# Performance work log

Hardware: AMD Instinct MI355X
Metric: run time of the kernel (lower is better)

## Reference

```python
import jax, jax.numpy as jnp
import numpy as np

NQ = 8
NL = 3
DIM = 2 ** NQ


def _rx(psi, w, theta):
    # theta: scalar or [B]
    B = psi.shape[0]
    t = jnp.atleast_1d(theta).astype(jnp.float32)
    c = jnp.cos(t / 2)[:, None, None].astype(jnp.complex64)
    s = (-1j * jnp.sin(t / 2))[:, None, None].astype(jnp.complex64)
    p = psi.reshape(B, 2 ** w, 2, -1)
    s0, s1 = p[:, :, 0], p[:, :, 1]
    return jnp.stack([c * s0 + s * s1, s * s0 + c * s1], axis=2).reshape(B, DIM)


def _ry(psi, w, theta):
    B = psi.shape[0]
    t = jnp.atleast_1d(theta).astype(jnp.float32)
    c = jnp.cos(t / 2)[:, None, None].astype(jnp.complex64)
    s = jnp.sin(t / 2)[:, None, None].astype(jnp.complex64)
    p = psi.reshape(B, 2 ** w, 2, -1)
    s0, s1 = p[:, :, 0], p[:, :, 1]
    return jnp.stack([c * s0 - s * s1, s * s0 + c * s1], axis=2).reshape(B, DIM)


def _rz(psi, w, theta):
    B = psi.shape[0]
    t = jnp.atleast_1d(theta).astype(jnp.float32)
    e0 = jnp.exp(-0.5j * t.astype(jnp.complex64))[:, None, None]
    e1 = jnp.exp(0.5j * t.astype(jnp.complex64))[:, None, None]
    p = psi.reshape(B, 2 ** w, 2, -1)
    return jnp.stack([e0 * p[:, :, 0], e1 * p[:, :, 1]], axis=2).reshape(B, DIM)


def _cnot(psi, c, t):
    # control c, target t (wire 0 = most significant axis)
    B = psi.shape[0]
    a, b = (c, t) if c < t else (t, c)
    p = psi.reshape(B, 2 ** a, 2, 2 ** (b - a - 1), 2, -1)
    caxis = 2 if c < t else 4
    taxis = 4 if c < t else 2
    idx = [slice(None)] * 6
    idx[caxis] = 1
    sub = p[tuple(idx)]  # control=1 slab, caxis removed
    fl_axis = taxis - (1 if taxis > caxis else 0)
    p = p.at[tuple(idx)].set(jnp.flip(sub, axis=fl_axis))
    return p.reshape(B, DIM)


# PauliZ signs per wire: [NQ, 2^NQ]
_bits = (np.arange(DIM)[None, :] >> (NQ - 1 - np.arange(NQ)[:, None])) & 1
_Z_SIGNS = jnp.asarray((1 - 2 * _bits).astype(np.float32))


def _quantum_layer(enc, qrx, qry, qrz):
    # enc: [B, NQ] encoding angles; qrx/qry/qrz: [NL, NQ] scalar params
    B = enc.shape[0]
    psi = jnp.zeros((B, DIM), jnp.complex64).at[:, 0].set(1.0)
    for i in range(NQ):
        psi = _rx(psi, i, enc[:, i])
    for l in range(NL):
        for i in range(NQ):
            psi = _rx(psi, i, qrx[l, i])
            psi = _ry(psi, i, qry[l, i])
            psi = _rz(psi, i, qrz[l, i])
        for i in range(NQ - 1):
            psi = _cnot(psi, i, i + 1)
        psi = _cnot(psi, NQ - 1, 0)
    probs = psi.real ** 2 + psi.imag ** 2  # [B, 2^NQ]
    return probs @ _Z_SIGNS.T  # [B, NQ] <Z_i>


def _critic(x, w1, b1, w2, b2, qrx, qry, qrz, w3, b3, w4, b4):
    h = jax.nn.relu(x @ w1 + b1)
    enc = h @ w2 + b2
    ex = _quantum_layer(enc, qrx, qry, qrz)
    h2 = jax.nn.relu(ex @ w3 + b3)
    return h2 @ w4 + b4


def setup_inputs() -> dict:
    key = jax.random.key(0)
    ks = jax.random.split(key, 32)
    B, OBS, ACT, H = 65536, 96, 32, 256
    D = OBS + ACT

    def lin(k, fin, fout):
        return jax.random.normal(k, (fin, fout), jnp.float32) * (1.0 / np.sqrt(fin))

    inp = {
        'state': jax.random.normal(ks[0], (B, OBS), jnp.float32),
        'action': jax.random.normal(ks[1], (B, ACT), jnp.float32),
    }
    for ci, tag in enumerate(['a', 'b']):
        o = 2 + ci * 15
        inp['w1' + tag] = lin(ks[o + 0], D, H)
        inp['b1' + tag] = jnp.zeros((H,), jnp.float32)
        inp['w2' + tag] = lin(ks[o + 1], H, NQ)
        inp['b2' + tag] = jnp.zeros((NQ,), jnp.float32)
        inp['qrx' + tag] = jax.random.normal(ks[o + 2], (NL, NQ), jnp.float32)
        inp['qry' + tag] = jax.random.normal(ks[o + 3], (NL, NQ), jnp.float32)
        inp['qrz' + tag] = jax.random.normal(ks[o + 4], (NL, NQ), jnp.float32)
        inp['w3' + tag] = lin(ks[o + 5], NQ, H)
        inp['b3' + tag] = jnp.zeros((H,), jnp.float32)
        inp['w4' + tag] = lin(ks[o + 6], H, 1)
        inp['b4' + tag] = jnp.zeros((1,), jnp.float32)
    return inp


def reference(state, action,
              w1a, b1a, w2a, b2a, qrxa, qrya, qrza, w3a, b3a, w4a, b4a,
              w1b, b1b, w2b, b2b, qrxb, qryb, qrzb, w3b, b3b, w4b, b4b):
    x = jnp.concatenate([state, action], axis=1)
    q1 = _critic(x, w1a, b1a, w2a, b2a, qrxa, qrya, qrza, w3a, b3a, w4a, b4a)
    q2 = _critic(x, w1b, b1b, w2b, b2b, qrxb, qryb, qrzb, w3b, b3b, w4b, b4b)
    return (q1, q2)
```

## Files before the change

### kernel.cpp

```cpp
#include <hip/hip_runtime.h>
#include <math.h>


typedef __attribute__((ext_vector_type(8))) short bfrag_t;
typedef __attribute__((ext_vector_type(16))) float accv_t;

__device__ __forceinline__ unsigned short f2bf(float x) {
  unsigned u = __float_as_uint(x);
  u += 0x7FFFu + ((u >> 16) & 1u);
  return (unsigned short)(u >> 16);
}
__device__ __forceinline__ float bf2f(unsigned short h) {
  return __uint_as_float(((unsigned)h) << 16);
}
__device__ __forceinline__ unsigned pack2(float a, float b) {
  return (unsigned)f2bf(a) | ((unsigned)f2bf(b) << 16);
}

struct C2 { float r, i; };
__device__ __forceinline__ C2 cmul(C2 a, C2 b){ return C2{a.r*b.r - a.i*b.i, a.r*b.i + a.i*b.r}; }
__device__ __forceinline__ C2 cadd(C2 a, C2 b){ return C2{a.r+b.r, a.i+b.i}; }

#define APPLY2(A,Bx)                                                        \
  { float ar=re[A], ai=im[A], br=re[Bx], bi=im[Bx];                         \
    re[A]  = u00r*ar - u00i*ai + u01r*br - u01i*bi;                         \
    im[A]  = u00r*ai + u00i*ar + u01r*bi + u01i*br;                         \
    re[Bx] = u10r*ar - u10i*ai + u11r*br - u11i*bi;                         \
    im[Bx] = u10r*ai + u10i*ar + u11r*bi + u11i*br; }

__global__ __launch_bounds__(256)
void prep_weights(const float* __restrict__ qrxa, const float* __restrict__ qrya,
                  const float* __restrict__ qrza,
                  const float* __restrict__ qrxb, const float* __restrict__ qryb,
                  const float* __restrict__ qrzb,
                  const float* __restrict__ w1a, const float* __restrict__ w1b,
                  const float* __restrict__ w2a, const float* __restrict__ w2b,
                  const float* __restrict__ w3a, const float* __restrict__ w3b,
                  unsigned short* __restrict__ Bm, unsigned short* __restrict__ Gm,
                  unsigned short* __restrict__ w1p, unsigned short* __restrict__ w2p) {
  int blk = blockIdx.x;
  int tid = threadIdx.x;
  if (blk < 128) {
    __shared__ float sg[192];
    int c = blk >> 6;
    if (tid < 24) {
      const float* qx = c ? qrxb : qrxa;
      const float* qy = c ? qryb : qrya;
      const float* qz = c ? qrzb : qrza;
      int g = tid;
      float tx = 0.5f*qx[g], ty = 0.5f*qy[g], tz = 0.5f*qz[g];
      float cx = cosf(tx), sx = sinf(tx);
      float cy = cosf(ty), sy = sinf(ty);
      float cz = cosf(tz), sz = sinf(tz);
      C2 rx00{cx,0.f}, rx01{0.f,-sx}, rx10{0.f,-sx}, rx11{cx,0.f};
      C2 m00 = cadd(cmul(C2{cy,0.f},rx00), cmul(C2{-sy,0.f},rx10));
      C2 m01 = cadd(cmul(C2{cy,0.f},rx01), cmul(C2{-sy,0.f},rx11));
      C2 m10 = cadd(cmul(C2{sy,0.f},rx00), cmul(C2{cy,0.f},rx10));
      C2 m11 = cadd(cmul(C2{sy,0.f},rx01), cmul(C2{cy,0.f},rx11));
      C2 e0{cz,-sz}, e1{cz,sz};
      C2 u00 = cmul(e0,m00), u01 = cmul(e0,m01), u10 = cmul(e1,m10), u11 = cmul(e1,m11);
      float* o = sg + g*8;
      o[0]=u00.r; o[1]=u00.i; o[2]=u01.r; o[3]=u01.i;
      o[4]=u10.r; o[5]=u10.i; o[6]=u11.r; o[7]=u11.i;
    }
    __syncthreads();
    int lane = tid & 63;
    int wid = blk*4 + (tid >> 6);
    int bcol = wid & 255;
    int p = __popc(bcol) & 3;
    float phr = (p==0) ? 1.f : ((p==2) ? -1.f : 0.f);
    float phi = (p==1) ? -1.f : ((p==3) ? 1.f : 0.f);
    float re[4], im[4];
    #pragma unroll
    for (int j = 0; j < 4; ++j) {
      int idx = 4*lane + j;
      re[j] = (idx==bcol) ? phr : 0.f;
      im[j] = (idx==bcol) ? phi : 0.f;
    }
    #pragma unroll
    for (int l = 0; l < 3; ++l) {
      #pragma unroll
      for (int q = 0; q < 8; ++q) {
        const float* u = &sg[(size_t)(l*8 + q)*8];
        float u00r=u[0],u00i=u[1],u01r=u[2],u01i=u[3];
        float u10r=u[4],u10i=u[5],u11r=u[6],u11i=u[7];
        if (q < 6) {
          int m = 5-q, mask = 1<<m;
          bool s1 = ((lane >> m) & 1) != 0;
          float udr = s1?u11r:u00r, udi = s1?u11i:u00i;
          float uor = s1?u10r:u01r, uoi = s1?u10i:u01i;
          #pragma unroll
          for (int j = 0; j < 4; ++j) {
            float pr = __shfl_xor(re[j], mask);
            float pi = __shfl_xor(im[j], mask);
            float nr = udr*re[j] - udi*im[j] + uor*pr - uoi*pi;
            float ni = udr*im[j] + udi*re[j] + uor*pi + uoi*pr;
            re[j]=nr; im[j]=ni;
          }
        } else if (q == 6) { APPLY2(0,2); APPLY2(1,3); }
        else               { APPLY2(0,1); APPLY2(2,3); }
      }
      #pragma unroll
      for (int cq = 0; cq <= 4; ++cq) {
        int tmask = 1 << (4-cq);
        bool pred = ((lane >> (5-cq)) & 1) != 0;
        #pragma unroll
        for (int j = 0; j < 4; ++j) {
          float sr = __shfl_xor(re[j], tmask);
          float si = __shfl_xor(im[j], tmask);
          re[j] = pred ? sr : re[j];
          im[j] = pred ? si : im[j];
        }
      }
      { bool pred = (lane & 1) != 0;
        float t0, t1;
        t0 = pred?re[2]:re[0]; t1 = pred?re[0]:re[2]; re[0]=t0; re[2]=t1;
        t0 = pred?im[2]:im[0]; t1 = pred?im[0]:im[2]; im[0]=t0; im[2]=t1;
        t0 = pred?re[3]:re[1]; t1 = pred?re[1]:re[3]; re[1]=t0; re[3]=t1;
        t0 = pred?im[3]:im[1]; t1 = pred?im[1]:im[3]; im[1]=t0; im[3]=t1; }
      { float t;
        t=re[2]; re[2]=re[3]; re[3]=t;
        t=im[2]; im[2]=im[3]; im[3]=t; }
      { re[1]=__shfl_xor(re[1],32); im[1]=__shfl_xor(im[1],32);
        re[3]=__shfl_xor(re[3],32); im[3]=__shfl_xor(im[3],32); }
    }
    #pragma unroll
    for (int j = 0; j < 4; ++j) {
      int i = 4*lane + j;
      Bm[(size_t)(c*512 + i)*256 + bcol]       = f2bf(re[j]);
      Bm[(size_t)(c*512 + 256 + i)*256 + bcol] = f2bf(im[j]);
    }
  } else if (blk < 192) {
    int slot = (blk-128)*256 + tid;
    int n = slot & 255, h5 = (slot>>8)&1, ks = (slot>>9)&7, p = (slot>>12)&1, c = slot>>13;
    const float* w1c = c ? w1b : w1a;
    #pragma unroll
    for (int j = 0; j < 8; ++j) {
      float v = w1c[(size_t)(ks*16 + h5*8 + j)*256 + n];
      unsigned short hi = f2bf(v);
      w1p[(size_t)slot*8 + j] = p ? f2bf(v - bf2f(hi)) : hi;
    }
  } else if (blk < 200) {
    int slot = (blk-192)*256 + tid;
    int combo = slot >> 4, part = slot & 15;
    int h5 = combo&1, k16 = (combo>>1)&15, p = (combo>>5)&1, c = (combo>>6)&1;
    const float* w2c = c ? w2b : w2a;
    #pragma unroll
    for (int jj = 0; jj < 16; ++jj) {
      int idx = part*16 + jj;
      int il = idx >> 3, j = idx & 7;
      int n = k16*16 + h5*8 + j;
      float v = (il < 8) ? w2c[(size_t)n*8 + il] : 0.f;
      unsigned short hi = f2bf(v);
      w2p[(size_t)combo*256 + idx] = p ? f2bf(v - bf2f(hi)) : hi;
    }
  } else {
    int idx = (blk-200)*256 + tid;
    int j = idx & 7, lane = (idx >> 3) & 63, w = (idx >> 9) & 7, c = (idx >> 12) & 1;
    int h5 = lane >> 5, il = lane & 31;
    int n = 32*w + il;
    const float* w3 = c ? w3b : w3a;
    Gm[idx] = h5 ? (unsigned short)0 : f2bf(w3[j*256 + n]);
  }
}

__global__ __launch_bounds__(256, 4)
void enc_mfma(const float* __restrict__ state, const float* __restrict__ action,
              const unsigned short* __restrict__ w1p,
              const float* __restrict__ b1a, const float* __restrict__ b1b,
              const unsigned short* __restrict__ w2p,
              const float* __restrict__ b2a, const float* __restrict__ b2b,
              float* __restrict__ enc, int Bn) {
  __shared__ __align__(16) char Bx[2][8192];
  __shared__ __align__(16) float sb1[2][256];
  __shared__ float sb2[2][8];
  __shared__ __align__(16) float encw[4][32][8];
  int tid = threadIdx.x;
  int lane = tid & 63, w = tid >> 6, il = lane & 31, h5 = lane >> 5;
  int r0 = blockIdx.x * 32;

  sb1[0][tid] = b1a[tid];
  sb1[1][tid] = b1b[tid];
  if (tid < 8) { sb2[0][tid] = b2a[tid]; sb2[1][tid] = b2b[tid]; }

  {
    int m = tid >> 3, q8 = tid & 7;
    const float4* st4 = (const float4*)state;
    const float4* ac4 = (const float4*)action;
    #pragma unroll
    for (int j = 0; j < 4; ++j) {
      int f = j*8 + q8;
      int ks = f >> 2, kq = f & 3;
      float4 v = (ks < 6) ? st4[(size_t)(r0+m)*24 + ks*4 + kq]
                          : ac4[(size_t)(r0+m)*8 + (ks-6)*4 + kq];
      unsigned short hx = f2bf(v.x), hy = f2bf(v.y), hz = f2bf(v.z), hw = f2bf(v.w);
      uint2 hh, ll;
      hh.x = (unsigned)hx | ((unsigned)hy << 16);
      hh.y = (unsigned)hz | ((unsigned)hw << 16);
      ll.x = (unsigned)f2bf(v.x - bf2f(hx)) | ((unsigned)f2bf(v.y - bf2f(hy)) << 16);
      ll.y = (unsigned)f2bf(v.z - bf2f(hz)) | ((unsigned)f2bf(v.w - bf2f(hw)) << 16);
      int off = ks*1024 + m*32 + kq*8;
      *(uint2*)(&Bx[0][off]) = hh;
      *(uint2*)(&Bx[1][off]) = ll;
    }
  }
  __syncthreads();

  for (int c = 0; c < 2; ++c) {
    accv_t A[2] = {{},{}};
    #pragma unroll
    for (int ks = 0; ks < 8; ++ks) {
      bfrag_t a0h, a0l, a1h, a1l;
      {
        size_t b0 = ((size_t)((c*2+0)*8 + ks)*2 + h5)*256;
        size_t b1 = ((size_t)((c*2+1)*8 + ks)*2 + h5)*256;
        int t0 = 2*w, t1 = 2*w+1;
        a0h = *(const bfrag_t*)(w1p + (b0 + t0*32 + il)*8);
        a0l = *(const bfrag_t*)(w1p + (b1 + t0*32 + il)*8);
        a1h = *(const bfrag_t*)(w1p + (b0 + t1*32 + il)*8);
        a1l = *(const bfrag_t*)(w1p + (b1 + t1*32 + il)*8);
      }
      bfrag_t b0h = *(const bfrag_t*)(&Bx[0][ks*1024 + il*32 + h5*16]);
      bfrag_t b0l = *(const bfrag_t*)(&Bx[1][ks*1024 + il*32 + h5*16]);
      A[0] = __builtin_amdgcn_mfma_f32_32x32x16_bf16(a0h, b0h, A[0], 0,0,0);
      A[0] = __builtin_amdgcn_mfma_f32_32x32x16_bf16(a0h, b0l, A[0], 0,0,0);
      A[0] = __builtin_amdgcn_mfma_f32_32x32x16_bf16(a0l, b0h, A[0], 0,0,0);
      A[1] = __builtin_amdgcn_mfma_f32_32x32x16_bf16(a1h, b0h, A[1], 0,0,0);
      A[1] = __builtin_amdgcn_mfma_f32_32x32x16_bf16(a1h, b0l, A[1], 0,0,0);
      A[1] = __builtin_amdgcn_mfma_f32_32x32x16_bf16(a1l, b0h, A[1], 0,0,0);
    }
    #pragma unroll
    for (int nt = 0; nt < 2; ++nt) {
      #pragma unroll
      for (int g = 0; g < 4; ++g) {
        float4 bb = *(const float4*)&sb1[c][(2*w+nt)*32 + 8*g + 4*h5];
        float bba[4] = {bb.x, bb.y, bb.z, bb.w};
        #pragma unroll
        for (int jj = 0; jj < 4; ++jj) {
          A[nt][4*g+jj] = fmaxf(A[nt][4*g+jj] + bba[jj], 0.f);
        }
      }
    }
    accv_t Cm = {};
    #pragma unroll
    for (int k2 = 0; k2 < 4; ++k2) {
      int k16 = 4*w + k2;
      bfrag_t g2h = *(const bfrag_t*)(w2p + ((size_t)((c*2+0)*16 + k16)*2 + h5)*256 + il*8);
      bfrag_t g2l = *(const bfrag_t*)(w2p + ((size_t)((c*2+1)*16 + k16)*2 + h5)*256 + il*8);
      unsigned ph[2][2], pl[2][2];
      #pragma unroll
      for (int gi = 0; gi < 2; ++gi) {
        int G = 2*k2 + gi, nt = G >> 2, g = G & 3;
        float f0 = A[nt][4*g+0], f1 = A[nt][4*g+1];
        float f2 = A[nt][4*g+2], f3 = A[nt][4*g+3];
        unsigned short h0 = f2bf(f0), h1 = f2bf(f1), h2 = f2bf(f2), h3 = f2bf(f3);
        ph[gi][0] = (unsigned)h0 | ((unsigned)h1 << 16);
        ph[gi][1] = (unsigned)h2 | ((unsigned)h3 << 16);
        pl[gi][0] = (unsigned)f2bf(f0 - bf2f(h0)) | ((unsigned)f2bf(f1 - bf2f(h1)) << 16);
        pl[gi][1] = (unsigned)f2bf(f2 - bf2f(h2)) | ((unsigned)f2bf(f3 - bf2f(h3)) << 16);
      }
      union { bfrag_t v; unsigned u[4]; } FH, FL;
      #pragma unroll
      for (int r = 0; r < 2; ++r) {
        unsigned own_h = h5 ? ph[1][r] : ph[0][r];
        unsigned alt_h = h5 ? ph[0][r] : ph[1][r];
        unsigned rec_h = __shfl_xor((int)alt_h, 32);
        FH.u[r]   = h5 ? rec_h : own_h;
        FH.u[2+r] = h5 ? own_h : rec_h;
        unsigned own_l = h5 ? pl[1][r] : pl[0][r];
        unsigned alt_l = h5 ? pl[0][r] : pl[1][r];
        unsigned rec_l = __shfl_xor((int)alt_l, 32);
        FL.u[r]   = h5 ? rec_l : own_l;
        FL.u[2+r] = h5 ? own_l : rec_l;
      }
      Cm = __builtin_amdgcn_mfma_f32_32x32x16_bf16(g2h, FH.v, Cm, 0,0,0);
      Cm = __builtin_amdgcn_mfma_f32_32x32x16_bf16(g2h, FL.v, Cm, 0,0,0);
      Cm = __builtin_amdgcn_mfma_f32_32x32x16_bf16(g2l, FH.v, Cm, 0,0,0);
    }
    *(float4*)&encw[w][il][4*h5] = make_float4(Cm[0], Cm[1], Cm[2], Cm[3]);
    __syncthreads();
    {
      int e = tid & 7, mm = tid >> 3;
      float v = sb2[c][e];
      #pragma unroll
      for (int ww = 0; ww < 4; ++ww) v += encw[ww][mm][e];
      enc[((size_t)c*Bn + r0 + mm)*8 + e] = v;
    }
    __syncthreads();
  }
}

__device__ __forceinline__ void a_build(float4 ea, float4 eb, char* Ab, int ag2, int am) {
  float c0,s0,c1,s1,c2,s2,c3,s3,c4,s4,c5,s5,c6,s6,c7,s7;
  __sincosf(0.5f*ea.x, &s0, &c0);
  __sincosf(0.5f*ea.y, &s1, &c1);
  __sincosf(0.5f*ea.z, &s2, &c2);
  __sincosf(0.5f*ea.w, &s3, &c3);
  __sincosf(0.5f*eb.x, &s4, &c4);
  __sincosf(0.5f*eb.y, &s5, &c5);
  __sincosf(0.5f*eb.z, &s6, &c6);
  __sincosf(0.5f*eb.w, &s7, &c7);
  float v0 = (ag2&8) ? s0 : c0;
  float v1 = (ag2&4) ? s1 : c1;
  float v2 = (ag2&2) ? s2 : c2;
  float v3 = (ag2&1) ? s3 : c3;
  float top = v0*v1*v2*v3;
  float hA = top*c4, hB = top*s4;
  float p67[4];
  p67[0] = c6*c7; p67[1] = c6*s7; p67[2] = s6*c7; p67[3] = s6*s7;
  float low[8];
  #pragma unroll
  for (int j = 0; j < 8; ++j) low[j] = ((j&4) ? s5 : c5) * p67[j&3];
  union { bfrag_t v; unsigned u[4]; } pk;
  #pragma unroll
  for (int k = 0; k < 4; ++k) pk.u[k] = pack2(hA*low[2*k], hA*low[2*k+1]);
  *(bfrag_t*)(Ab + ag2*1024 + am*16) = pk.v;
  #pragma unroll
  for (int k = 0; k < 4; ++k) pk.u[k] = pack2(hB*low[2*k], hB*low[2*k+1]);
  *(bfrag_t*)(Ab + ag2*1024 + 512 + am*16) = pk.v;
}

__global__ __launch_bounds__(512, 2)
void qgemm(const float* __restrict__ enc,
           const unsigned short* __restrict__ Bm, const unsigned short* __restrict__ Gm,
           const float* __restrict__ b3a, const float* __restrict__ w4a, const float* __restrict__ b4a,
           const float* __restrict__ b3b, const float* __restrict__ w4b, const float* __restrict__ b4b,
           float* __restrict__ out, int Bn) {
  __shared__ __align__(16) char APq[119808];
  char* A0 = APq;
  char* A1 = APq + 16384;
  float* exw = (float*)(APq + 32768);
  float* exf = (float*)(APq + 51200);
  float* qtmp = (float*)(APq + 54272);

  int tid = threadIdx.x;
  int lane = tid & 63;
  int w = tid >> 6;
  int il = lane & 31;
  int h5 = lane >> 5;

  int c = blockIdx.x >> 7;
  int rowblock = blockIdx.x & 127;
  int rowsPerBlock = Bn >> 7;
  int npairs = rowsPerBlock >> 6;

  bfrag_t bf0[16], bf1[16];
  {
    const unsigned short* base = Bm + ((size_t)(c*512 + 32*w + il)*256 + h5*8);
    #pragma unroll
    for (int ks = 0; ks < 16; ++ks) {
      bf0[ks] = *(const bfrag_t*)(base + ks*16);
      bf1[ks] = *(const bfrag_t*)(base + 256*256 + ks*16);
    }
  }
  bfrag_t gf2 = *(const bfrag_t*)(Gm + ((size_t)((c*8 + w)*64 + lane))*8);

  int n2 = 32*w + il;
  const float* b3c = c ? b3b : b3a;
  const float* w4c = c ? w4b : w4a;
  const float* b4c = c ? b4b : b4a;
  float b3v = b3c[n2];
  float w4v = w4c[n2];
  float b4v = b4c[0];
  int rowAdd = 4*h5;

  int am = tid & 31, ag2 = tid >> 5;
  const float* encb = enc + ((size_t)c*Bn)*8;
  int rbase = rowblock*rowsPerBlock;

  {
    const float* ep0 = encb + (size_t)(rbase + am)*8;
    float4 pa0 = *(const float4*)ep0, pb0 = *(const float4*)(ep0 + 4);
    const float* ep1 = encb + (size_t)(rbase + 32 + am)*8;
    float4 pa1 = *(const float4*)ep1, pb1 = *(const float4*)(ep1 + 4);
    a_build(pa0, pb0, A0, ag2, am);
    a_build(pa1, pb1, A1, ag2, am);
  }
  __syncthreads();

  for (int st2 = 0; st2 < npairs; ++st2) {
    int r0 = rbase + st2*64;
    #pragma unroll
    for (int sub = 0; sub < 2; ++sub) {
      const char* Asel = sub ? A1 : A0;
      accv_t acc0 = {}, acc1 = {};
      #pragma unroll
      for (int ks = 0; ks < 16; ++ks) {
        bfrag_t af = *(const bfrag_t*)(Asel + ks*1024 + lane*16);
        acc0 = __builtin_amdgcn_mfma_f32_32x32x16_bf16(bf0[ks], af, acc0, 0, 0, 0);
        acc1 = __builtin_amdgcn_mfma_f32_32x32x16_bf16(bf1[ks], af, acc1, 0, 0, 0);
      }
      float Pv[16];
      #pragma unroll
      for (int r = 0; r < 16; ++r) Pv[r] = acc0[r]*acc0[r] + acc1[r]*acc1[r];
      float E  = ((Pv[0]+Pv[1])+(Pv[2]+Pv[3])) + ((Pv[4]+Pv[5])+(Pv[6]+Pv[7]));
      float S4 = ((Pv[8]+Pv[9])+(Pv[10]+Pv[11])) + ((Pv[12]+Pv[13])+(Pv[14]+Pv[15]));
      float T  = E + S4;
      float S0 = ((Pv[1]+Pv[3])+(Pv[5]+Pv[7])) + ((Pv[9]+Pv[11])+(Pv[13]+Pv[15]));
      float S1 = ((Pv[2]+Pv[3])+(Pv[6]+Pv[7])) + ((Pv[10]+Pv[11])+(Pv[14]+Pv[15]));
      float S3 = ((Pv[4]+Pv[5])+(Pv[6]+Pv[7])) + ((Pv[12]+Pv[13])+(Pv[14]+Pv[15]));
      float e[8];
      e[7] = T - 2.f*S0;
      e[6] = T - 2.f*S1;
      e[5] = h5 ? -T : T;
      e[4] = T - 2.f*S3;
      e[3] = T - 2.f*S4;
      e[2] = (w&1) ? -T : T;
      e[1] = (w&2) ? -T : T;
      e[0] = (w&4) ? -T : T;
      #pragma unroll
      for (int q = 0; q < 8; ++q) e[q] += __shfl_xor(e[q], 32);
      if (h5 == 0) {
        float* dst = exw + sub*2304 + w*288 + il*9;
        #pragma unroll
        for (int q = 0; q < 8; ++q) dst[q] = e[q];
      }
    }
    __syncthreads();
    float4 na0, nb0, na1, nb1;
    bool more = (st2 + 1 < npairs);
    if (more) {
      const float* ep0 = encb + (size_t)(r0 + 64 + am)*8;
      na0 = *(const float4*)ep0; nb0 = *(const float4*)(ep0 + 4);
      const float* ep1 = encb + (size_t)(r0 + 96 + am)*8;
      na1 = *(const float4*)ep1; nb1 = *(const float4*)(ep1 + 4);
    }
    {
      int sub = tid >> 8, m = (tid >> 3) & 31, q = tid & 7;
      const float* ew = exw + sub*2304 + m*9 + q;
      float s = ((ew[0] + ew[288]) + (ew[2*288] + ew[3*288]))
              + ((ew[4*288] + ew[5*288]) + (ew[6*288] + ew[7*288]));
      exf[sub*384 + m*12 + q] = s;
    }
    if (more) {
      a_build(na0, nb0, A0, ag2, am);
      a_build(na1, nb1, A1, ag2, am);
    }
    __syncthreads();
    {
      union { bfrag_t v; unsigned u[4]; } fa, fb;
      if (h5 == 0) {
        const float* e0 = exf + il*12;
        float4 x0 = *(const float4*)(e0);
        float4 x1 = *(const float4*)(e0 + 4);
        fa.u[0] = pack2(x0.x, x0.y); fa.u[1] = pack2(x0.z, x0.w);
        fa.u[2] = pack2(x1.x, x1.y); fa.u[3] = pack2(x1.z, x1.w);
        const float* e1 = exf + 384 + il*12;
        float4 y0 = *(const float4*)(e1);
        float4 y1 = *(const float4*)(e1 + 4);
        fb.u[0] = pack2(y0.x, y0.y); fb.u[1] = pack2(y0.z, y0.w);
        fb.u[2] = pack2(y1.x, y1.y); fb.u[3] = pack2(y1.z, y1.w);
      } else {
        fa.u[0]=0; fa.u[1]=0; fa.u[2]=0; fa.u[3]=0;
        fb.u[0]=0; fb.u[1]=0; fb.u[2]=0; fb.u[3]=0;
      }
      accv_t acc2a = {}, acc2b = {};
      acc2a = __builtin_amdgcn_mfma_f32_32x32x16_bf16(fa.v, gf2, acc2a, 0, 0, 0);
      acc2b = __builtin_amdgcn_mfma_f32_32x32x16_bf16(fb.v, gf2, acc2b, 0, 0, 0);
      #pragma unroll
      for (int r = 0; r < 16; ++r) {
        int row = (r&3) + 8*(r>>2) + rowAdd;
        qtmp[row*256 + n2]        = fmaxf(acc2a[r] + b3v, 0.f) * w4v;
        qtmp[(32 + row)*256 + n2] = fmaxf(acc2b[r] + b3v, 0.f) * w4v;
      }
    }
    __syncthreads();
    {
      int row = tid >> 3, seg = tid & 7;
      const float* qrow = qtmp + row*256;
      float s = 0.f;
      #pragma unroll
      for (int t = 0; t < 8; ++t) {
        float4 a = *(const float4*)(qrow + t*32 + seg*4);
        s += (a.x + a.y) + (a.z + a.w);
      }
      s += __shfl_xor(s, 1);
      s += __shfl_xor(s, 2);
      s += __shfl_xor(s, 4);
      if (seg == 0) out[(size_t)c*Bn + r0 + row] = s + b4v;
    }
  }
}

extern "C" void kernel_launch(void* const* d_in, const int* in_sizes, int n_in,
                              void* d_out, int out_size, void* d_ws, size_t ws_size,
                              hipStream_t stream) {
  (void)n_in; (void)out_size; (void)ws_size;
  const float* state  = (const float*)d_in[0];
  const float* action = (const float*)d_in[1];
  const float* w1a=(const float*)d_in[2];  const float* b1a=(const float*)d_in[3];
  const float* w2a=(const float*)d_in[4];  const float* b2a=(const float*)d_in[5];
  const float* qrxa=(const float*)d_in[6]; const float* qrya=(const float*)d_in[7];
  const float* qrza=(const float*)d_in[8];
  const float* w3a=(const float*)d_in[9];  const float* b3a=(const float*)d_in[10];
  const float* w4a=(const float*)d_in[11]; const float* b4a=(const float*)d_in[12];
  const float* w1b=(const float*)d_in[13]; const float* b1b=(const float*)d_in[14];
  const float* w2b=(const float*)d_in[15]; const float* b2b=(const float*)d_in[16];
  const float* qrxb=(const float*)d_in[17];const float* qryb=(const float*)d_in[18];
  const float* qrzb=(const float*)d_in[19];
  const float* w3b=(const float*)d_in[20]; const float* b3b=(const float*)d_in[21];
  const float* w4b=(const float*)d_in[22]; const float* b4b=(const float*)d_in[23];

  int B = in_sizes[0] / 96;
  char* wsb = (char*)d_ws;
  unsigned short* Bmat = (unsigned short*)(wsb);
  unsigned short* Gmat = (unsigned short*)(wsb + 524288);
  unsigned short* w1p  = (unsigned short*)(wsb + 786432);
  unsigned short* w2p  = (unsigned short*)(wsb + 1048576);
  float* enc           = (float*)(wsb + 1114112);

  prep_weights<<<232, 256, 0, stream>>>(qrxa,qrya,qrza,qrxb,qryb,qrzb,
                                        w1a,w1b,w2a,w2b,w3a,w3b,
                                        Bmat,Gmat,w1p,w2p);
  enc_mfma<<<B/32, 256, 0, stream>>>(state,action,w1p,b1a,b1b,w2p,b2a,b2b,enc,B);
  qgemm<<<256, 512, 0, stream>>>(enc, Bmat, Gmat, b3a, w4a, b4a, b3b, w4b, b4b,
                                 (float*)d_out, B);
}
```

Baseline: 204.2 us.

## Fold w4 magnitude and b3 into Gm, reduce head in registers

```diff
diff --git a/kernel.cpp b/kernel.cpp
--- a/kernel.cpp
+++ b/kernel.cpp
@@ -36,6 +36,8 @@
                   const float* __restrict__ w1a, const float* __restrict__ w1b,
                   const float* __restrict__ w2a, const float* __restrict__ w2b,
                   const float* __restrict__ w3a, const float* __restrict__ w3b,
+                  const float* __restrict__ w4a, const float* __restrict__ w4b,
+                  const float* __restrict__ b3a, const float* __restrict__ b3b,
                   unsigned short* __restrict__ Bm, unsigned short* __restrict__ Gm,
                   unsigned short* __restrict__ w1p, unsigned short* __restrict__ w2p) {
   int blk = blockIdx.x;
@@ -160,7 +162,14 @@
     int h5 = lane >> 5, il = lane & 31;
     int n = 32*w + il;
     const float* w3 = c ? w3b : w3a;
-    Gm[idx] = h5 ? (unsigned short)0 : f2bf(w3[j*256 + n]);
+    const float* w4 = c ? w4b : w4a;
+    const float* b3 = c ? b3b : b3a;
+    float aw = fabsf(w4[n]);
+    float v;
+    if (h5 == 0)     v = w3[(size_t)j*256 + n] * aw;
+    else if (j == 0) v = b3[n] * aw;
+    else             v = 0.f;
+    Gm[idx] = f2bf(v);
   }
 }
 
@@ -326,12 +335,12 @@
            const float* __restrict__ b3a, const float* __restrict__ w4a, const float* __restrict__ b4a,
            const float* __restrict__ b3b, const float* __restrict__ w4b, const float* __restrict__ b4b,
            float* __restrict__ out, int Bn) {
-  __shared__ __align__(16) char APq[119808];
+  __shared__ __align__(16) char APq[56576];
   char* A0 = APq;
   char* A1 = APq + 16384;
   float* exw = (float*)(APq + 32768);
   float* exf = (float*)(APq + 51200);
-  float* qtmp = (float*)(APq + 54272);
+  float* qp  = (float*)(APq + 54272);
 
   int tid = threadIdx.x;
   int lane = tid & 63;
@@ -356,13 +365,11 @@
   bfrag_t gf2 = *(const bfrag_t*)(Gm + ((size_t)((c*8 + w)*64 + lane))*8);
 
   int n2 = 32*w + il;
-  const float* b3c = c ? b3b : b3a;
   const float* w4c = c ? w4b : w4a;
   const float* b4c = c ? b4b : b4a;
-  float b3v = b3c[n2];
   float w4v = w4c[n2];
   float b4v = b4c[0];
-  int rowAdd = 4*h5;
+  unsigned smask = (unsigned)__ballot(w4v < 0.f);
 
   int am = tid & 31, ag2 = tid >> 5;
   const float* encb = enc + ((size_t)c*Bn)*8;
@@ -417,6 +424,11 @@
       }
     }
     __syncthreads();
+    if (st2 > 0 && tid < 64) {
+      const float* qr = qp + tid*9;
+      float s = ((qr[0]+qr[1]) + (qr[2]+qr[3])) + ((qr[4]+qr[5]) + (qr[6]+qr[7]));
+      out[(size_t)c*Bn + (r0 - 64) + tid] = s + b4v;
+    }
     float4 na0, nb0, na1, nb1;
     bool more = (st2 + 1 < npairs);
     if (more) {
@@ -451,34 +463,35 @@
         fb.u[0] = pack2(y0.x, y0.y); fb.u[1] = pack2(y0.z, y0.w);
         fb.u[2] = pack2(y1.x, y1.y); fb.u[3] = pack2(y1.z, y1.w);
       } else {
-        fa.u[0]=0; fa.u[1]=0; fa.u[2]=0; fa.u[3]=0;
-        fb.u[0]=0; fb.u[1]=0; fb.u[2]=0; fb.u[3]=0;
+        fa.u[0] = 0x00003F80u; fa.u[1]=0; fa.u[2]=0; fa.u[3]=0;
+        fb.u[0] = 0x00003F80u; fb.u[1]=0; fb.u[2]=0; fb.u[3]=0;
       }
       accv_t acc2a = {}, acc2b = {};
-      acc2a = __builtin_amdgcn_mfma_f32_32x32x16_bf16(fa.v, gf2, acc2a, 0, 0, 0);
-      acc2b = __builtin_amdgcn_mfma_f32_32x32x16_bf16(fb.v, gf2, acc2b, 0, 0, 0);
+      acc2a = __builtin_amdgcn_mfma_f32_32x32x16_bf16(gf2, fa.v, acc2a, 0, 0, 0);
+      acc2b = __builtin_amdgcn_mfma_f32_32x32x16_bf16(gf2, fb.v, acc2b, 0, 0, 0);
+      float qa = 0.f, qb = 0.f;
       #pragma unroll
       for (int r = 0; r < 16; ++r) {
-        int row = (r&3) + 8*(r>>2) + rowAdd;
-        qtmp[row*256 + n2]        = fmaxf(acc2a[r] + b3v, 0.f) * w4v;
-        qtmp[(32 + row)*256 + n2] = fmaxf(acc2b[r] + b3v, 0.f) * w4v;
-      }
-    }
-    __syncthreads();
-    {
-      int row = tid >> 3, seg = tid & 7;
-      const float* qrow = qtmp + row*256;
-      float s = 0.f;
-      #pragma unroll
-      for (int t = 0; t < 8; ++t) {
-        float4 a = *(const float4*)(qrow + t*32 + seg*4);
-        s += (a.x + a.y) + (a.z + a.w);
-      }
-      s += __shfl_xor(s, 1);
-      s += __shfl_xor(s, 2);
-      s += __shfl_xor(s, 4);
-      if (seg == 0) out[(size_t)c*Bn + r0 + row] = s + b4v;
-    }
+        int bi = (r&3) + 8*(r>>2);
+        float ta = fmaxf(acc2a[r], 0.f);
+        float tb = fmaxf(acc2b[r], 0.f);
+        bool neg = ((smask >> (bi + 4*h5)) & 1u) != 0u;
+        qa += neg ? -ta : ta;
+        qb += neg ? -tb : tb;
+      }
+      qa += __shfl_xor(qa, 32);
+      qb += __shfl_xor(qb, 32);
+      if (h5 == 0) {
+        qp[il*9 + w]        = qa;
+        qp[(32 + il)*9 + w] = qb;
+      }
+    }
+  }
+  __syncthreads();
+  if (tid < 64) {
+    const float* qr = qp + tid*9;
+    float s = ((qr[0]+qr[1]) + (qr[2]+qr[3])) + ((qr[4]+qr[5]) + (qr[6]+qr[7]));
+    out[(size_t)c*Bn + rbase + (npairs-1)*64 + tid] = s + b4v;
   }
 }
 
@@ -510,7 +523,7 @@
   float* enc           = (float*)(wsb + 1114112);
 
   prep_weights<<<232, 256, 0, stream>>>(qrxa,qrya,qrza,qrxb,qryb,qrzb,
-                                        w1a,w1b,w2a,w2b,w3a,w3b,
+                                        w1a,w1b,w2a,w2b,w3a,w3b,w4a,w4b,b3a,b3b,
                                         Bmat,Gmat,w1p,w2p);
   enc_mfma<<<B/32, 256, 0, stream>>>(state,action,w1p,b1a,b1b,w2p,b2a,b2b,enc,B);
   qgemm<<<256, 512, 0, stream>>>(enc, Bmat, Gmat, b3a, w4a, b4a, b3b, w4b, b4b,
```

Result: no change. 203.0 us (-0.6%).
